# Optimization experiments

Hardware: AMD Instinct MI355X
Metric: run time of the kernel (lower is better)

Reference implementation:

```python
import jax, jax.numpy as jnp
import numpy as np

NEG_INF = -1e9  # same masked_fill constant as the torch module
ALPHA = 0.1     # LeakyReLU negative slope


def setup_inputs() -> dict:
    key = jax.random.key(0)
    k1, k2, k3, k4, k5 = jax.random.split(key, 5)
    B, N, Din, Dout = 8, 2048, 512, 512
    features = jax.random.normal(k1, (B, N, Din), dtype=jnp.float32)
    graph = jax.random.randint(k2, (B, N, N), 0, 2, dtype=jnp.int64)
    # xavier_uniform with gain=1.414: limit = gain*sqrt(6/(fan_in+fan_out))
    lim_w = 1.414 * np.sqrt(6.0 / (Din + Dout))
    w = jax.random.uniform(k3, (Din, Dout), jnp.float32, -lim_w, lim_w)
    lim_a = 1.414 * np.sqrt(6.0 / (Dout + 1))
    a1 = jax.random.uniform(k4, (Dout, 1), jnp.float32, -lim_a, lim_a)
    a2 = jax.random.uniform(k5, (Dout, 1), jnp.float32, -lim_a, lim_a)
    return {"features": features, "graph": graph, "w": w, "a1": a1, "a2": a2}


def reference(features, graph, w, a1, a2):
    # hidden: [B, N, Dout]
    hidden = jnp.einsum("bni,io->bno", features, w)
    s1 = hidden @ a1  # [B, N, 1] -> broadcasts over columns
    s2 = hidden @ a2  # [B, N, 1] -> transposed broadcasts over rows
    # e[b,i,j] = leaky_relu(s1[b,i] + s2[b,j])
    e = jax.nn.leaky_relu(s1 + jnp.swapaxes(s2, 1, 2), negative_slope=ALPHA)
    e = jnp.where(graph == 0, NEG_INF, e)
    attn = jax.nn.softmax(e, axis=-1)  # [B, N, N]; dropout p=0 -> identity
    h_prime = jnp.einsum("bij,bjo->bio", attn, hidden)
    return jax.nn.elu(h_prime)  # concat=True
```

## Files before the change

### kernel.cpp

```cpp
#include <hip/hip_runtime.h>
#include <math.h>

#define B_ 8
#define N_ 2048
#define D_ 512
#define NROWS (B_ * N_)
#define NEG_ALPHA 0.1f

typedef __bf16 bf16;
typedef __bf16 bf16x4 __attribute__((ext_vector_type(4)));
typedef __bf16 bf16x8 __attribute__((ext_vector_type(8)));
typedef float f32x4 __attribute__((ext_vector_type(4)));
typedef float f32x16 __attribute__((ext_vector_type(16)));

#define HTB_BATCH ((D_ / 32) * (N_ / 16) * 512)

__global__ __launch_bounds__(256) void k_prep(const float* __restrict__ W,
                                              bf16* __restrict__ Wt) {
  __shared__ float tile[64][65];
  const int din0 = blockIdx.y * 64, dout0 = blockIdx.x * 64;
  const int tx = threadIdx.x & 63, tg = threadIdx.x >> 6;
#pragma unroll
  for (int rr = 0; rr < 16; ++rr) {
    int dr = tg * 16 + rr;
    tile[dr][tx] = W[(size_t)(din0 + dr) * D_ + dout0 + tx];
  }
  __syncthreads();
#pragma unroll
  for (int rr = 0; rr < 4; ++rr) {
    int dl = rr * 16 + (threadIdx.x >> 4);
    int nl = (threadIdx.x & 15) * 4;
    bf16x4 v = {(bf16)tile[nl][dl], (bf16)tile[nl + 1][dl],
                (bf16)tile[nl + 2][dl], (bf16)tile[nl + 3][dl]};
    *(bf16x4*)&Wt[(size_t)(dout0 + dl) * D_ + din0 + nl] = v;
  }
}

__global__ __launch_bounds__(256) void k_wa(const float* __restrict__ W,
                                            const float* __restrict__ a1,
                                            const float* __restrict__ a2,
                                            float* __restrict__ wa1,
                                            float* __restrict__ wa2) {
  const int wv = threadIdx.x >> 6, lane = threadIdx.x & 63;
  const int row = blockIdx.x * 4 + wv;
  const float* wr = W + (size_t)row * D_;
  float d1 = 0.f, d2 = 0.f;
#pragma unroll
  for (int p = 0; p < 8; ++p) {
    int c = lane + p * 64;
    float w = wr[c];
    d1 = fmaf(w, a1[c], d1);
    d2 = fmaf(w, a2[c], d2);
  }
#pragma unroll
  for (int off = 32; off > 0; off >>= 1) {
    d1 += __shfl_down(d1, off, 64);
    d2 += __shfl_down(d2, off, 64);
  }
  if (lane == 0) {
    wa1[row] = d1;
    wa2[row] = d2;
  }
}

__global__ __launch_bounds__(256) void k_scores_x(const float* __restrict__ X,
                                                  const float* __restrict__ wa1,
                                                  const float* __restrict__ wa2,
                                                  float* __restrict__ s1,
                                                  float* __restrict__ s2,
                                                  bf16* __restrict__ Xb) {
  const int wv = threadIdx.x >> 6, lane = threadIdx.x & 63;
  const int r = blockIdx.x * 4 + wv;
  const float* x = X + (size_t)r * D_;
  float d1 = 0.f, d2 = 0.f;
#pragma unroll
  for (int p = 0; p < 2; ++p) {
    int c = lane * 4 + p * 256;
    float4 xv = *(const float4*)&x[c];
    float4 w1 = *(const float4*)&wa1[c];
    float4 w2 = *(const float4*)&wa2[c];
    d1 += xv.x * w1.x + xv.y * w1.y + xv.z * w1.z + xv.w * w1.w;
    d2 += xv.x * w2.x + xv.y * w2.y + xv.z * w2.z + xv.w * w2.w;
    bf16x4 h = {(bf16)xv.x, (bf16)xv.y, (bf16)xv.z, (bf16)xv.w};
    *(bf16x4*)&Xb[(size_t)r * D_ + c] = h;
  }
#pragma unroll
  for (int off = 32; off > 0; off >>= 1) {
    d1 += __shfl_down(d1, off, 64);
    d2 += __shfl_down(d2, off, 64);
  }
  if (lane == 0) {
    s1[r] = d1;
    s2[r] = d2;
  }
}

__global__ __launch_bounds__(256) void k_gpack(const int* __restrict__ G,
                                               unsigned int* __restrict__ GB) {
  const size_t g = (size_t)blockIdx.x * 256 + threadIdx.x;
  const int* src = G + g * 32;
  unsigned int bits = 0;
#pragma unroll
  for (int p = 0; p < 8; ++p) {
    int4 v = *(const int4*)&src[p * 4];
    bits |= (unsigned)(v.x != 0) << (p * 4);
    bits |= (unsigned)(v.y != 0) << (p * 4 + 1);
    bits |= (unsigned)(v.z != 0) << (p * 4 + 2);
    bits |= (unsigned)(v.w != 0) << (p * 4 + 3);
  }
  GB[g] = bits;
}

#define LDH 40

__global__ __launch_bounds__(256, 2) void k_hiddenT(const bf16* __restrict__ Xb,
                                                    const bf16* __restrict__ Wt,
                                                    bf16* __restrict__ HtB) {
  __shared__ bf16 As[128][LDH];
  __shared__ bf16 Bs[128][LDH];
  const int t = threadIdx.x;
  const int m0 = blockIdx.y * 128;
  const int n0 = blockIdx.x * 128;
  const int lane = t & 63, w = t >> 6;
  const int wm = w >> 1, wn = w & 1;
  const int l15 = lane & 15, q = lane >> 4;

  f32x4 acc[4][4];
#pragma unroll
  for (int i = 0; i < 4; ++i)
#pragma unroll
    for (int j = 0; j < 4; ++j) acc[i][j] = (f32x4){0.f, 0.f, 0.f, 0.f};

  bf16x8 av[2], bv[2];
#pragma unroll
  for (int p = 0; p < 2; ++p) {
    int s = t + p * 256;
    av[p] = *(const bf16x8*)&Wt[(size_t)(m0 + (s >> 2)) * D_ + (s & 3) * 8];
    bv[p] = *(const bf16x8*)&Xb[(size_t)(n0 + (s >> 2)) * D_ + (s & 3) * 8];
  }

  for (int k0 = 0; k0 < D_; k0 += 32) {
    __syncthreads();
#pragma unroll
    for (int p = 0; p < 2; ++p) {
      int s = t + p * 256;
      *(bf16x8*)&As[s >> 2][(s & 3) * 8] = av[p];
      *(bf16x8*)&Bs[s >> 2][(s & 3) * 8] = bv[p];
    }
    __syncthreads();
    if (k0 + 32 < D_) {
#pragma unroll
      for (int p = 0; p < 2; ++p) {
        int s = t + p * 256;
        av[p] = *(const bf16x8*)&Wt[(size_t)(m0 + (s >> 2)) * D_ + k0 + 32 + (s & 3) * 8];
        bv[p] = *(const bf16x8*)&Xb[(size_t)(n0 + (s >> 2)) * D_ + k0 + 32 + (s & 3) * 8];
      }
    }
    bf16x8 a[4], bb[4];
#pragma unroll
    for (int i = 0; i < 4; ++i)
      a[i] = *(const bf16x8*)&As[wm * 64 + i * 16 + l15][q * 8];
#pragma unroll
    for (int j = 0; j < 4; ++j)
      bb[j] = *(const bf16x8*)&Bs[wn * 64 + j * 16 + l15][q * 8];
#pragma unroll
    for (int i = 0; i < 4; ++i)
#pragma unroll
      for (int j = 0; j < 4; ++j)
        acc[i][j] =
            __builtin_amdgcn_mfma_f32_16x16x32_bf16(a[i], bb[j], acc[i][j], 0, 0, 0);
  }
#pragma unroll
  for (int i = 0; i < 4; ++i)
#pragma unroll
    for (int r = 0; r < 4; ++r) {
      int dout = m0 + wm * 64 + i * 16 + q * 4 + r;
#pragma unroll
      for (int j = 0; j < 4; ++j) {
        int row = n0 + wn * 64 + j * 16 + l15;
        int bb_ = row >> 11;
        int jj = row & (N_ - 1);
        size_t addr = (size_t)bb_ * HTB_BATCH +
                      ((size_t)((dout >> 5) * (N_ / 16) + (jj >> 4)) * 64 +
                       ((jj >> 3) & 1) * 32 + (dout & 31)) *
                          8 +
                      (jj & 7);
        HtB[addr] = (bf16)acc[i][j][r];
      }
    }
}

#define AT_BM 64
#define AT_BK 64
#define LDP 72
#define NIT (N_ / AT_BK)
#define GROW 272

#define ATTN_BODY(PS, BC, BN, IT)                                              \
  {                                                                            \
    const int j0_ = (IT)*AT_BK;                                                \
    unsigned gbyte = gb_s[pi][(IT)*8 + (t & 7)];                               \
    float pv[8];                                                               \
    {                                                                          \
      f32x4 sA = *(const f32x4*)&s2s[j0_ + pj];                                \
      f32x4 sB = *(const f32x4*)&s2s[j0_ + pj + 4];                            \
      float sv[8] = {sA.x, sA.y, sA.z, sA.w, sB.x, sB.y, sB.z, sB.w};          \
      _Pragma("unroll") for (int q_ = 0; q_ < 8; ++q_) {                       \
        float e = s1r + sv[q_];                                                \
        e = (e > 0.f) ? e : NEG_ALPHA * e;                                     \
        pv[q_] = ((gbyte >> q_) & 1) ? __expf(e) : 0.f;                        \
        rsum += pv[q_];                                                        \
      }                                                                        \
    }                                                                          \
    {                                                                          \
      bf16x8 pb = {(bf16)pv[0], (bf16)pv[1], (bf16)pv[2], (bf16)pv[3],         \
                   (bf16)pv[4], (bf16)pv[5], (bf16)pv[6], (bf16)pv[7]};        \
      *(bf16x8*)&Ps[PS][pi][pj] = pb;                                          \
    }                                                                          \
    __syncthreads();            \
    {               \
      int j0n = ((IT) + 1 < NIT) ? ((IT) + 1) * AT_BK : 0;                     \
      _Pragma("unroll") for (int nt = 0; nt < 2; ++nt)                         \
          _Pragma("unroll") for (int ks = 0; ks < 4; ++ks)                     \
              BN[nt][ks] = *(const bf16x8*)&Hb[(size_t)((                      \
                  ((w * 2 + nt) * (N_ / 16) + (j0n >> 4) + ks) * 64 + lane))   \
                  * 8];                                                        \
    }                                                                          \
    _Pragma("unroll") for (int ks = 0; ks < 4; ++ks) {                         \
      const int ko = ks * 16 + hf * 8;                                         \
      bf16x8 a0 = *(const bf16x8*)&Ps[PS][r31][ko];                            \
      bf16x8 a1 = *(const bf16x8*)&Ps[PS][32 + r31][ko];                       \
      acc[0][0] = __builtin_amdgcn_mfma_f32_32x32x16_bf16(a0, BC[0][ks],       \
                                                          acc[0][0], 0, 0, 0); \
      acc[0][1] = __builtin_amdgcn_mfma_f32_32x32x16_bf16(a0, BC[1][ks],       \
                                                          acc[0][1], 0, 0, 0); \
      acc[1][0] = __builtin_amdgcn_mfma_f32_32x32x16_bf16(a1, BC[0][ks],       \
                                                          acc[1][0], 0, 0, 0); \
      acc[1][1] = __builtin_amdgcn_mfma_f32_32x32x16_bf16(a1, BC[1][ks],       \
                                                          acc[1][1], 0, 0, 0); \
    }                                                                          \
  }

__global__ __launch_bounds__(512) void k_attn(const bf16* __restrict__ HtB,
                                              const unsigned char* __restrict__ GB,
                                              const float* __restrict__ s1,
                                              const float* __restrict__ s2,
                                              float* __restrict__ out) {
  __shared__ __align__(16) bf16 Ps[2][AT_BM][LDP];
  __shared__ float s2s[N_];
  __shared__ __align__(16) unsigned char gb_s[AT_BM][GROW];
  __shared__ float sum_part[AT_BM][8];
  __shared__ float row_sum[AT_BM];

  const int t = threadIdx.x;
  const int bid = blockIdx.x;
  const int b = bid & 7;
  const int i0 = (bid >> 3) * AT_BM;
  const int lane = t & 63, w = t >> 6;
  const int r31 = lane & 31, hf = lane >> 5;

  const bf16* Hb = HtB + (size_t)b * HTB_BATCH;
  const unsigned char* GBb = GB + ((size_t)b * N_ + i0) * (N_ / 8);

  for (int c = t; c < N_; c += 512) s2s[c] = s2[b * N_ + c];
  {
    int gr = t >> 3, gc = (t & 7) * 32;
    int4 w0 = *(const int4*)&GBb[(size_t)gr * (N_ / 8) + gc];
    int4 w1 = *(const int4*)&GBb[(size_t)gr * (N_ / 8) + gc + 16];
    *(int4*)&gb_s[gr][gc] = w0;
    *(int4*)&gb_s[gr][gc + 16] = w1;
  }

  const int pi = t >> 3;
  const int pj = (t & 7) * 8;
  const float s1r = s1[b * N_ + i0 + pi];
  float rsum = 0.f;

  f32x16 acc[2][2];
#pragma unroll
  for (int i = 0; i < 2; ++i)
#pragma unroll
    for (int j = 0; j < 2; ++j)
#pragma unroll
      for (int r = 0; r < 16; ++r) acc[i][j][r] = 0.f;

  bf16x8 bA[2][4], bB[2][4];
#pragma unroll
  for (int nt = 0; nt < 2; ++nt)
#pragma unroll
    for (int ks = 0; ks < 4; ++ks)
      bA[nt][ks] = *(const bf16x8*)&Hb[(size_t)(
          ((w * 2 + nt) * (N_ / 16) + ks) * 64 + lane) * 8];

  __syncthreads();

#pragma unroll 1
  for (int i2 = 0; i2 < NIT / 2; ++i2) {
    const int it0 = i2 * 2;
    ATTN_BODY(0, bA, bB, it0);
    ATTN_BODY(1, bB, bA, it0 + 1);
  }

  sum_part[pi][t & 7] = rsum;
  __syncthreads();
  if (t < AT_BM) {
    float s = 0.f;
#pragma unroll
    for (int k = 0; k < 8; ++k) s += sum_part[t][k];
    row_sum[t] = s;
  }
  __syncthreads();

#pragma unroll
  for (int mt = 0; mt < 2; ++mt) {
    float inv[16];
#pragma unroll
    for (int r = 0; r < 16; ++r)
      inv[r] = 1.f / row_sum[mt * 32 + (r & 3) + 8 * (r >> 2) + 4 * hf];
#pragma unroll
    for (int nt = 0; nt < 2; ++nt) {
      const int d = w * 64 + nt * 32 + r31;
#pragma unroll
      for (int r = 0; r < 16; ++r) {
        int i = mt * 32 + (r & 3) + 8 * (r >> 2) + 4 * hf;
        float x = acc[mt][nt][r] * inv[r];
        out[((size_t)b * N_ + i0 + i) * D_ + d] = (x > 0.f) ? x : expm1f(x);
      }
    }
  }
}

extern "C" void kernel_launch(void* const* d_in, const int* in_sizes, int n_in,
                              void* d_out, int out_size, void* d_ws,
                              size_t ws_size, hipStream_t stream) {
  const float* X = (const float*)d_in[0];
  const int* graph = (const int*)d_in[1];
  const float* W = (const float*)d_in[2];
  const float* a1 = (const float*)d_in[3];
  const float* a2 = (const float*)d_in[4];
  float* out = (float*)d_out;

  char* ws = (char*)d_ws;
  bf16* Wt = (bf16*)ws;
  bf16* HtB = (bf16*)(ws + (1 << 19));
  bf16* Xb = (bf16*)(ws + (1 << 19) + (16 << 20));
  unsigned int* GBw = (unsigned int*)(ws + (1 << 19) + (32 << 20));
  float* s1 = (float*)(ws + (1 << 19) + (37 << 20));
  float* s2 = s1 + NROWS;
  float* wa1 = s2 + NROWS;
  float* wa2 = wa1 + D_;

  hipLaunchKernelGGL(k_prep, dim3(8, 8), dim3(256), 0, stream, W, Wt);
  hipLaunchKernelGGL(k_wa, dim3(128), dim3(256), 0, stream, W, a1, a2, wa1, wa2);
  hipLaunchKernelGGL(k_scores_x, dim3(NROWS / 4), dim3(256), 0, stream, X, wa1,
                     wa2, s1, s2, Xb);
  hipLaunchKernelGGL(k_gpack, dim3((B_ * N_ * N_) / (256 * 32)), dim3(256), 0,
                     stream, graph, GBw);
  hipLaunchKernelGGL(k_hiddenT, dim3(NROWS / 128, D_ / 128), dim3(256), 0,
                     stream, Xb, Wt, HtB);
  hipLaunchKernelGGL(k_attn, dim3(N_ / AT_BM * B_), dim3(512), 0, stream, HtB,
                     (const unsigned char*)GBw, s1, s2, out);
}
```

Before: 299.3 us.

## Fuse graph bit-packing into score kernel and use direct global-to-LDS loads in GEMM

Folds the graph adjacency bit-packing into the per-row score/bf16-convert kernel, removing one launch. This works because both grids have NROWS/4 blocks of 256 threads. The hidden-projection GEMM now uses global_load_lds to fill unpadded 128x64 LDS tiles directly, with a K step of 64. It drops the register-staged prefetch and raises the occupancy hint to 3 blocks. The trade-off is losing the register double-buffer overlap, and the unpadded LDS layout may cause bank conflicts on fragment reads.

```diff
diff --git a/kernel.cpp b/kernel.cpp
--- a/kernel.cpp
+++ b/kernel.cpp
@@ -68,7 +68,9 @@
                                                   const float* __restrict__ wa2,
                                                   float* __restrict__ s1,
                                                   float* __restrict__ s2,
-                                                  bf16* __restrict__ Xb) {
+                                                  bf16* __restrict__ Xb,
+                                                  const int* __restrict__ G,
+                                                  unsigned int* __restrict__ GB) {
   const int wv = threadIdx.x >> 6, lane = threadIdx.x & 63;
   const int r = blockIdx.x * 4 + wv;
   const float* x = X + (size_t)r * D_;
@@ -84,6 +86,20 @@
     bf16x4 h = {(bf16)xv.x, (bf16)xv.y, (bf16)xv.z, (bf16)xv.w};
     *(bf16x4*)&Xb[(size_t)r * D_ + c] = h;
   }
+  {
+    const size_t g = (size_t)blockIdx.x * 256 + threadIdx.x;
+    const int* src = G + g * 32;
+    unsigned int bits = 0;
+#pragma unroll
+    for (int p = 0; p < 8; ++p) {
+      int4 v = *(const int4*)&src[p * 4];
+      bits |= (unsigned)(v.x != 0) << (p * 4);
+      bits |= (unsigned)(v.y != 0) << (p * 4 + 1);
+      bits |= (unsigned)(v.z != 0) << (p * 4 + 2);
+      bits |= (unsigned)(v.w != 0) << (p * 4 + 3);
+    }
+    GB[g] = bits;
+  }
 #pragma unroll
   for (int off = 32; off > 0; off >>= 1) {
     d1 += __shfl_down(d1, off, 64);
@@ -95,29 +111,11 @@
   }
 }
 
-__global__ __launch_bounds__(256) void k_gpack(const int* __restrict__ G,
-                                               unsigned int* __restrict__ GB) {
-  const size_t g = (size_t)blockIdx.x * 256 + threadIdx.x;
-  const int* src = G + g * 32;
-  unsigned int bits = 0;
-#pragma unroll
-  for (int p = 0; p < 8; ++p) {
-    int4 v = *(const int4*)&src[p * 4];
-    bits |= (unsigned)(v.x != 0) << (p * 4);
-    bits |= (unsigned)(v.y != 0) << (p * 4 + 1);
-    bits |= (unsigned)(v.z != 0) << (p * 4 + 2);
-    bits |= (unsigned)(v.w != 0) << (p * 4 + 3);
-  }
-  GB[g] = bits;
-}
-
-#define LDH 40
-
-__global__ __launch_bounds__(256, 2) void k_hiddenT(const bf16* __restrict__ Xb,
+__global__ __launch_bounds__(256, 3) void k_hiddenT(const bf16* __restrict__ Xb,
                                                     const bf16* __restrict__ Wt,
                                                     bf16* __restrict__ HtB) {
-  __shared__ bf16 As[128][LDH];
-  __shared__ bf16 Bs[128][LDH];
+  __shared__ bf16 As[128 * 64];
+  __shared__ bf16 Bs[128 * 64];
   const int t = threadIdx.x;
   const int m0 = blockIdx.y * 128;
   const int n0 = blockIdx.x * 128;
@@ -131,44 +129,40 @@
 #pragma unroll
     for (int j = 0; j < 4; ++j) acc[i][j] = (f32x4){0.f, 0.f, 0.f, 0.f};
 
-  bf16x8 av[2], bv[2];
-#pragma unroll
-  for (int p = 0; p < 2; ++p) {
-    int s = t + p * 256;
-    av[p] = *(const bf16x8*)&Wt[(size_t)(m0 + (s >> 2)) * D_ + (s & 3) * 8];
-    bv[p] = *(const bf16x8*)&Xb[(size_t)(n0 + (s >> 2)) * D_ + (s & 3) * 8];
-  }
-
-  for (int k0 = 0; k0 < D_; k0 += 32) {
+  const int scol = (lane & 7) * 8;
+
+  for (int k0 = 0; k0 < D_; k0 += 64) {
+#pragma unroll
+    for (int p = 0; p < 4; ++p) {
+      const int rbase = w * 32 + p * 8;
+      const int row = rbase + (lane >> 3);
+      __builtin_amdgcn_global_load_lds(
+          (const __attribute__((address_space(1))) void*)
+              &Wt[(size_t)(m0 + row) * D_ + k0 + scol],
+          (__attribute__((address_space(3))) void*)&As[rbase * 64], 16, 0, 0);
+      __builtin_amdgcn_global_load_lds(
+          (const __attribute__((address_space(1))) void*)
+              &Xb[(size_t)(n0 + row) * D_ + k0 + scol],
+          (__attribute__((address_space(3))) void*)&Bs[rbase * 64], 16, 0, 0);
+    }
     __syncthreads();
 #pragma unroll
-    for (int p = 0; p < 2; ++p) {
-      int s = t + p * 256;
-      *(bf16x8*)&As[s >> 2][(s & 3) * 8] = av[p];
-      *(bf16x8*)&Bs[s >> 2][(s & 3) * 8] = bv[p];
+    for (int kc = 0; kc < 2; ++kc) {
+      bf16x8 a[4], bb[4];
+#pragma unroll
+      for (int i = 0; i < 4; ++i)
+        a[i] = *(const bf16x8*)&As[(wm * 64 + i * 16 + l15) * 64 + kc * 32 + q * 8];
+#pragma unroll
+      for (int j = 0; j < 4; ++j)
+        bb[j] = *(const bf16x8*)&Bs[(wn * 64 + j * 16 + l15) * 64 + kc * 32 + q * 8];
+#pragma unroll
+      for (int i = 0; i < 4; ++i)
+#pragma unroll
+        for (int j = 0; j < 4; ++j)
+          acc[i][j] = __builtin_amdgcn_mfma_f32_16x16x32_bf16(a[i], bb[j],
+                                                              acc[i][j], 0, 0, 0);
     }
     __syncthreads();
-    if (k0 + 32 < D_) {
-#pragma unroll
-      for (int p = 0; p < 2; ++p) {
-        int s = t + p * 256;
-        av[p] = *(const bf16x8*)&Wt[(size_t)(m0 + (s >> 2)) * D_ + k0 + 32 + (s & 3) * 8];
-        bv[p] = *(const bf16x8*)&Xb[(size_t)(n0 + (s >> 2)) * D_ + k0 + 32 + (s & 3) * 8];
-      }
-    }
-    bf16x8 a[4], bb[4];
-#pragma unroll
-    for (int i = 0; i < 4; ++i)
-      a[i] = *(const bf16x8*)&As[wm * 64 + i * 16 + l15][q * 8];
-#pragma unroll
-    for (int j = 0; j < 4; ++j)
-      bb[j] = *(const bf16x8*)&Bs[wn * 64 + j * 16 + l15][q * 8];
-#pragma unroll
-    for (int i = 0; i < 4; ++i)
-#pragma unroll
-      for (int j = 0; j < 4; ++j)
-        acc[i][j] =
-            __builtin_amdgcn_mfma_f32_16x16x32_bf16(a[i], bb[j], acc[i][j], 0, 0, 0);
   }
 #pragma unroll
   for (int i = 0; i < 4; ++i)
@@ -353,9 +347,7 @@
   hipLaunchKernelGGL(k_prep, dim3(8, 8), dim3(256), 0, stream, W, Wt);
   hipLaunchKernelGGL(k_wa, dim3(128), dim3(256), 0, stream, W, a1, a2, wa1, wa2);
   hipLaunchKernelGGL(k_scores_x, dim3(NROWS / 4), dim3(256), 0, stream, X, wa1,
-                     wa2, s1, s2, Xb);
-  hipLaunchKernelGGL(k_gpack, dim3((B_ * N_ * N_) / (256 * 32)), dim3(256), 0,
-                     stream, graph, GBw);
+                     wa2, s1, s2, Xb, graph, GBw);
   hipLaunchKernelGGL(k_hiddenT, dim3(NROWS / 128, D_ / 128), dim3(256), 0,
                      stream, Xb, Wt, HtB);
   hipLaunchKernelGGL(k_attn, dim3(N_ / AT_BM * B_), dim3(512), 0, stream, HtB,
```

Result: slower. 305.4 us (+2.0%).
